# Kernel optimization log

Hardware: AMD Instinct MI355X
Metric: run time of the kernel (lower is better)

Reference implementation:

```python
import jax, jax.numpy as jnp
import numpy as np

S, B, E, H = 2048, 4, 512, 8
HD = E // H


def setup_inputs() -> dict:
    key = jax.random.key(0)
    ks = jax.random.split(key, 5)
    scale = 1.0 / np.sqrt(E)
    return {
        "query": jax.random.normal(ks[0], (S, B, E), jnp.float32),
        "key": jax.random.normal(ks[1], (S, B, E), jnp.float32),
        "value": jax.random.normal(ks[2], (S, B, E), jnp.float32),
        "in_proj_weight": jax.random.normal(ks[3], (3 * E, E), jnp.float32) * scale,
        "in_proj_bias": jnp.zeros((3 * E,), jnp.float32),
        "out_proj_weight": jax.random.normal(ks[4], (E, E), jnp.float32) * scale,
        "out_proj_bias": jnp.zeros((E,), jnp.float32),
    }


def reference(query, key, value, in_proj_weight, in_proj_bias, out_proj_weight, out_proj_bias):
    tgt_len, bsz, embed_dim = query.shape
    src_len = key.shape[0]
    # Quirk of this module: first chunk (w_qk) projects BOTH q and k; third chunk projects v.
    w_qk = in_proj_weight[:embed_dim]
    w_v = in_proj_weight[2 * embed_dim:]
    b_qk = in_proj_bias[:embed_dim]
    b_v = in_proj_bias[2 * embed_dim:]
    q = query @ w_qk.T + b_qk          # [S, B, E]
    k = key @ w_qk.T + b_qk
    v = value @ w_v.T + b_v
    # (S, B, E) -> (B*H, S, HD)
    def split_heads(x, n):
        return x.reshape(n, bsz * H, HD).transpose(1, 0, 2)
    q = split_heads(q, tgt_len) / jnp.sqrt(jnp.asarray(HD, q.dtype))
    k = split_heads(k, src_len)
    v = split_heads(v, src_len)
    scores = jnp.einsum("bqd,bkd->bqk", q, k)          # [B*H, S, S] full score matrix
    attn = jax.nn.softmax(scores, axis=-1)
    out = jnp.einsum("bqk,bkd->bqd", attn, v)          # [B*H, S, HD]
    out = out.transpose(1, 0, 2).reshape(tgt_len * bsz, embed_dim)
    out = out @ out_proj_weight.T + out_proj_bias
    return out.reshape(tgt_len, bsz, embed_dim)
```

## Files before the change

### kernel.cpp

```cpp
#include <hip/hip_runtime.h>
#include <hip/hip_bf16.h>

typedef __attribute__((ext_vector_type(8))) short s16x8;
typedef __attribute__((ext_vector_type(4))) short s16x4;
typedef __attribute__((ext_vector_type(4))) float f32x4;

#if __has_builtin(__builtin_amdgcn_exp2f)
#define EXP2F(x) __builtin_amdgcn_exp2f(x)
#else
#define EXP2F(x) exp2f(x)
#endif

#define S_LEN 2048
#define EMB   512
#define MROWS 8192

__device__ __forceinline__ float bf2f(short x) {
    union { float f; unsigned u; } z; z.u = ((unsigned)(unsigned short)x) << 16; return z.f;
}
__device__ __forceinline__ short f2bf(float f) {
    union { float f; unsigned u; } z; z.f = f;
    unsigned r = z.u + 0x7FFF + ((z.u >> 16) & 1);
    return (short)(r >> 16);
}
__device__ __forceinline__ short f2bf_fast(float f) {
    union { float f; unsigned u; } z; z.f = f;
    return (short)((z.u + 0x8000u) >> 16);
}

template<int AF32, int BF32>
__device__ __forceinline__ void gemm_mainloop(const void* __restrict__ Ag,
                                              const void* __restrict__ Bg,
                                              short* sA, short* sB,
                                              f32x4 acc[2][4], int K)
{
    const int tid  = threadIdx.x;
    const int lane = tid & 63;
    const int wv   = tid >> 6;
    const int l15  = lane & 15, quad = lane >> 4;
    const int wm   = (wv >> 1) * 32, wn = (wv & 1) * 64;

    f32x4 afr[2], bfr[2];
    s16x8 ahr, bhr;

    auto loadT = [&](const void* G, int kt, f32x4* fr, s16x8& hr, int F32) {
        if (F32) {
#pragma unroll
            for (int p = 0; p < 2; ++p) {
                int c = tid + p * 512;
                fr[p] = *(const f32x4*)((const float*)G + (size_t)(c >> 3) * K + kt + (c & 7) * 4);
            }
        } else {
            hr = *(const s16x8*)((const short*)G + (size_t)(tid >> 2) * K + kt + (tid & 3) * 8);
        }
    };
    auto commitT = [&](short* s, f32x4* fr, s16x8& hr, int F32) {
        if (F32) {
#pragma unroll
            for (int p = 0; p < 2; ++p) {
                int c = tid + p * 512;
                s16x4 o4;
                o4[0] = f2bf_fast(fr[p][0]); o4[1] = f2bf_fast(fr[p][1]);
                o4[2] = f2bf_fast(fr[p][2]); o4[3] = f2bf_fast(fr[p][3]);
                *(s16x4*)(s + c * 4) = o4;
            }
        } else {
            *(s16x8*)(s + tid * 8) = hr;
        }
    };

    loadT(Ag, 0, afr, ahr, AF32);
    loadT(Bg, 0, bfr, bhr, BF32);
    commitT(sA, afr, ahr, AF32);
    commitT(sB, bfr, bhr, BF32);
    __syncthreads();

    int cur = 0;
    for (int kt = 0; kt < K; kt += 32) {
        const int ktn = (kt + 32 < K) ? kt + 32 : 0;
        loadT(Ag, ktn, afr, ahr, AF32);
        loadT(Bg, ktn, bfr, bhr, BF32);

        const short* sAc = sA + cur * 4096;
        const short* sBc = sB + cur * 4096;
        s16x8 aF[2], bF[4];
#pragma unroll
        for (int i = 0; i < 2; ++i)
            aF[i] = *(const s16x8*)(sAc + (wm + i * 16 + l15) * 32 + quad * 8);
#pragma unroll
        for (int j = 0; j < 4; ++j)
            bF[j] = *(const s16x8*)(sBc + (wn + j * 16 + l15) * 32 + quad * 8);
#pragma unroll
        for (int i = 0; i < 2; ++i)
#pragma unroll
            for (int j = 0; j < 4; ++j)
                acc[i][j] = __builtin_amdgcn_mfma_f32_16x16x32_bf16(aF[i], bF[j], acc[i][j], 0, 0, 0);

        commitT(sA + (cur ^ 1) * 4096, afr, ahr, AF32);
        commitT(sB + (cur ^ 1) * 4096, bfr, bhr, BF32);
        __syncthreads();
        cur ^= 1;
    }
}

__global__ __launch_bounds__(512, 4) void qkv_proj(const float* __restrict__ query,
                                                   const float* __restrict__ key,
                                                   const float* __restrict__ value,
                                                   const float* __restrict__ W,
                                                   const float* __restrict__ bias,
                                                   short* __restrict__ q,
                                                   short* __restrict__ k,
                                                   short* __restrict__ vt)
{
    __shared__ __align__(16) short sA[2 * 4096], sB[2 * 4096];
    const int z = blockIdx.z;
    const float* X  = (z == 0) ? query : (z == 1) ? key : value;
    const float* Wz = W    + (z == 2 ? (size_t)1024 * EMB : 0);
    const float* bz = bias + (z == 2 ? 1024 : 0);
    const float scale = (z == 0) ? 0.125f * 1.44269504f : 1.0f;

    const int blockM = blockIdx.x * 128, blockN = blockIdx.y * 128;

    f32x4 acc[2][4];
#pragma unroll
    for (int i = 0; i < 2; ++i)
#pragma unroll
        for (int j = 0; j < 4; ++j)
            acc[i][j] = (f32x4){0.f, 0.f, 0.f, 0.f};

    gemm_mainloop<1, 1>(X + (size_t)blockM * EMB, Wz + (size_t)blockN * EMB,
                        sA, sB, acc, EMB);

    const int tid = threadIdx.x, lane = tid & 63, wv = tid >> 6;
    const int l15 = lane & 15, quad = lane >> 4;
    const int wm = (wv >> 1) * 32, wn = (wv & 1) * 64;

#pragma unroll
    for (int j = 0; j < 4; ++j) {
        int col = blockN + wn + j * 16 + l15;
        float bval = bz[col];
        int h = col >> 6, hd = col & 63;
#pragma unroll
        for (int i = 0; i < 2; ++i) {
#pragma unroll
            for (int r = 0; r < 4; ++r) {
                int row = blockM + wm + i * 16 + quad * 4 + r;
                int s = row >> 2, b = row & 3;
                float val = (acc[i][j][r] + bval) * scale;
                int bh = b * 8 + h;
                if (z == 2) {
                    vt[((size_t)(bh * 64 + hd)) * 2048 + s] = f2bf(val);
                } else {
                    short* dst = (z == 0) ? q : k;
                    dst[((size_t)(bh * 2048 + s)) * 64 + hd] = f2bf(val);
                }
            }
        }
    }
}

__global__ __launch_bounds__(256, 4) void flash_attn(const short* __restrict__ q,
                                                     const short* __restrict__ k,
                                                     const short* __restrict__ vt,
                                                     short* __restrict__ attn)
{
    __shared__ __align__(16) short sK[2][64 * 72];
    __shared__ __align__(16) short sV[2][64 * 72];
    const int bh = blockIdx.x;
    const int q0 = blockIdx.y * 64;
    const int tid = threadIdx.x, wv = tid >> 6, lane = tid & 63;
    const int l15 = lane & 15, quad = lane >> 4;

    const short* qp = q + ((size_t)(bh * 2048 + q0 + wv * 16 + l15)) * 64 + quad * 8;
    s16x8 qf0 = *(const s16x8*)qp;
    s16x8 qf1 = *(const s16x8*)(qp + 32);

    const short* kg = k  + (size_t)bh * 2048 * 64;
    const short* vg = vt + (size_t)bh * 64 * 2048;

    const int r0 = tid >> 3,          c0 = (tid & 7) * 8;
    const int r1 = (tid + 256) >> 3,  c1 = ((tid + 256) & 7) * 8;
    const int p0 = (r0 & 35) | ((r0 & 24) >> 1) | ((r0 & 4) << 2);
    const int p1 = (r1 & 35) | ((r1 & 24) >> 1) | ((r1 & 4) << 2);

    f32x4 o[4];
    float ls[4];
#pragma unroll
    for (int i = 0; i < 4; ++i) { o[i] = (f32x4){0.f, 0.f, 0.f, 0.f}; ls[i] = 0.f; }

    s16x8 ka = *(const s16x8*)(kg + (size_t)r0 * 64 + c0);
    s16x8 kb = *(const s16x8*)(kg + (size_t)r1 * 64 + c1);
    s16x8 va = *(const s16x8*)(vg + (size_t)r0 * 2048 + c0);
    s16x8 vb = *(const s16x8*)(vg + (size_t)r1 * 2048 + c1);
    *(s16x8*)(sK[0] + p0 * 72 + c0) = ka;
    *(s16x8*)(sK[0] + p1 * 72 + c1) = kb;
    *(s16x8*)(sV[0] + r0 * 72 + c0) = va;
    *(s16x8*)(sV[0] + r1 * 72 + c1) = vb;
    __syncthreads();

    int cur = 0;
    for (int kt = 0; kt < 2048; kt += 64) {
        const int ktn = (kt + 64) & 2047;
        ka = *(const s16x8*)(kg + (size_t)(ktn + r0) * 64 + c0);
        kb = *(const s16x8*)(kg + (size_t)(ktn + r1) * 64 + c1);
        va = *(const s16x8*)(vg + (size_t)r0 * 2048 + ktn + c0);
        vb = *(const s16x8*)(vg + (size_t)r1 * 2048 + ktn + c1);

        const short* Kc = sK[cur];
        const short* Vc = sV[cur];

        f32x4 sc[4];
#pragma unroll
        for (int ct = 0; ct < 4; ++ct) {
            s16x8 kf0 = *(const s16x8*)(Kc + (ct * 16 + l15) * 72 + quad * 8);
            s16x8 kf1 = *(const s16x8*)(Kc + (ct * 16 + l15) * 72 + quad * 8 + 32);
            f32x4 c = (f32x4){0.f, 0.f, 0.f, 0.f};
            c = __builtin_amdgcn_mfma_f32_16x16x32_bf16(kf0, qf0, c, 0, 0, 0);
            c = __builtin_amdgcn_mfma_f32_16x16x32_bf16(kf1, qf1, c, 0, 0, 0);
            sc[ct] = c;
        }
        s16x8 pf[2];
#pragma unroll
        for (int c = 0; c < 2; ++c)
#pragma unroll
            for (int h = 0; h < 2; ++h)
#pragma unroll
                for (int r = 0; r < 4; ++r) {
                    float p = EXP2F(sc[2 * c + h][r]);
                    ls[r] += p;
                    pf[c][h * 4 + r] = f2bf_fast(p);
                }
#pragma unroll
        for (int nt = 0; nt < 4; ++nt)
#pragma unroll
            for (int c = 0; c < 2; ++c) {
                s16x8 vf = *(const s16x8*)(Vc + (nt * 16 + l15) * 72 + c * 32 + quad * 8);
                o[nt] = __builtin_amdgcn_mfma_f32_16x16x32_bf16(pf[c], vf, o[nt], 0, 0, 0);
            }
        short* Kn = sK[cur ^ 1];
        short* Vn = sV[cur ^ 1];
        *(s16x8*)(Kn + p0 * 72 + c0) = ka;
        *(s16x8*)(Kn + p1 * 72 + c1) = kb;
        *(s16x8*)(Vn + r0 * 72 + c0) = va;
        *(s16x8*)(Vn + r1 * 72 + c1) = vb;
        __syncthreads();
        cur ^= 1;
    }

    float s = ls[0] + ls[1] + ls[2] + ls[3];
    s += __shfl_xor(s, 16, 64);
    s += __shfl_xor(s, 32, 64);
    float sinv = 1.0f / s;
    float inv[4];
#pragma unroll
    for (int r = 0; r < 4; ++r)
        inv[r] = __shfl(sinv, quad * 20 + r, 64);

    const int b = bh >> 3, h = bh & 7;
#pragma unroll
    for (int r = 0; r < 4; ++r) {
        int srow = q0 + wv * 16 + quad * 4 + r;
#pragma unroll
        for (int nt = 0; nt < 4; ++nt)
            attn[(size_t)(srow * 4 + b) * 512 + h * 64 + nt * 16 + l15] = f2bf(o[nt][r] * inv[r]);
    }
}

__global__ __launch_bounds__(512, 4) void out_proj(const short* __restrict__ attn,
                                                   const float* __restrict__ W,
                                                   const float* __restrict__ bias,
                                                   float* __restrict__ out)
{
    __shared__ __align__(16) short sA[2 * 4096], sB[2 * 4096];
    const int blockM = blockIdx.x * 128, blockN = blockIdx.y * 128;

    f32x4 acc[2][4];
#pragma unroll
    for (int i = 0; i < 2; ++i)
#pragma unroll
        for (int j = 0; j < 4; ++j)
            acc[i][j] = (f32x4){0.f, 0.f, 0.f, 0.f};

    gemm_mainloop<0, 1>(attn + (size_t)blockM * EMB, W + (size_t)blockN * EMB,
                        sA, sB, acc, EMB);

    const int tid = threadIdx.x, lane = tid & 63, wv = tid >> 6;
    const int l15 = lane & 15, quad = lane >> 4;
    const int wm = (wv >> 1) * 32, wn = (wv & 1) * 64;

#pragma unroll
    for (int j = 0; j < 4; ++j) {
        int col = blockN + wn + j * 16 + l15;
        float bval = bias[col];
#pragma unroll
        for (int i = 0; i < 2; ++i) {
#pragma unroll
            for (int r = 0; r < 4; ++r) {
                int row = blockM + wm + i * 16 + quad * 4 + r;
                out[(size_t)row * 512 + col] = acc[i][j][r] + bval;
            }
        }
    }
}

extern "C" void kernel_launch(void* const* d_in, const int* in_sizes, int n_in,
                              void* d_out, int out_size, void* d_ws, size_t ws_size,
                              hipStream_t stream)
{
    const float* query = (const float*)d_in[0];
    const float* key   = (const float*)d_in[1];
    const float* value = (const float*)d_in[2];
    const float* ipw   = (const float*)d_in[3];
    const float* ipb   = (const float*)d_in[4];
    const float* opw   = (const float*)d_in[5];
    const float* opb   = (const float*)d_in[6];
    float* out = (float*)d_out;

    const size_t NELEM = (size_t)MROWS * EMB;
    short* q    = (short*)d_ws;
    short* k    = q + NELEM;
    short* attn = k + NELEM;
    short* vt   = (short*)d_out;

    qkv_proj  <<<dim3(64, 4, 3), 512, 0, stream>>>(query, key, value, ipw, ipb, q, k, vt);
    flash_attn<<<dim3(32, 32),   256, 0, stream>>>(q, k, vt, attn);
    out_proj  <<<dim3(64, 4),    512, 0, stream>>>(attn, opw, opb, out);
}
```

Baseline: 205.5 us.

## Double query rows per attention wave and stage QKV epilogue through shared memory

```diff
diff --git a/kernel.cpp b/kernel.cpp
--- a/kernel.cpp
+++ b/kernel.cpp
@@ -112,7 +112,10 @@
                                                    short* __restrict__ k,
                                                    short* __restrict__ vt)
 {
-    __shared__ __align__(16) short sA[2 * 4096], sB[2 * 4096];
+    __shared__ __align__(16) short smem[16384];
+    short* sA = smem;
+    short* sB = smem + 8192;
+
     const int z = blockIdx.z;
     const float* X  = (z == 0) ? query : (z == 1) ? key : value;
     const float* Wz = W    + (z == 2 ? (size_t)1024 * EMB : 0);
@@ -137,29 +140,43 @@
 
 #pragma unroll
     for (int j = 0; j < 4; ++j) {
-        int col = blockN + wn + j * 16 + l15;
-        float bval = bz[col];
-        int h = col >> 6, hd = col & 63;
+        int colL = wn + j * 16 + l15;
+        float bval = bz[blockN + colL];
+        int hL = colL >> 6, hd = colL & 63;
 #pragma unroll
         for (int i = 0; i < 2; ++i) {
 #pragma unroll
             for (int r = 0; r < 4; ++r) {
-                int row = blockM + wm + i * 16 + quad * 4 + r;
-                int s = row >> 2, b = row & 3;
+                int rowL = wm + i * 16 + quad * 4 + r;
+                int b = rowL & 3, sp = rowL >> 2;
                 float val = (acc[i][j][r] + bval) * scale;
-                int bh = b * 8 + h;
-                if (z == 2) {
-                    vt[((size_t)(bh * 64 + hd)) * 2048 + s] = f2bf(val);
-                } else {
-                    short* dst = (z == 0) ? q : k;
-                    dst[((size_t)(bh * 2048 + s)) * 64 + hd] = f2bf(val);
-                }
-            }
-        }
-    }
-}
-
-__global__ __launch_bounds__(256, 4) void flash_attn(const short* __restrict__ q,
+                int idx = (z == 2) ? (((b * 2 + hL) * 64 + hd) * 32 + sp)
+                                   : (((b * 2 + hL) * 32 + sp) * 64 + hd);
+                smem[idx] = f2bf(val);
+            }
+        }
+    }
+    __syncthreads();
+
+    const s16x8* src = (const s16x8*)(smem + tid * 32);
+    if (z == 2) {
+        int b = tid >> 7, hL = (tid >> 6) & 1, hd = tid & 63;
+        int h = (blockN >> 6) + hL;
+        short* dst = vt + ((size_t)(b * 8 + h) * 64 + hd) * 2048 + (blockM >> 2);
+#pragma unroll
+        for (int u = 0; u < 4; ++u) ((s16x8*)dst)[u] = src[u];
+    } else {
+        int b = tid >> 7, hL = (tid >> 6) & 1;
+        int sp = (tid >> 1) & 31, hdh = (tid & 1) * 32;
+        int h = (blockN >> 6) + hL;
+        short* dstp = (z == 0) ? q : k;
+        short* dst = dstp + ((size_t)(b * 8 + h) * 2048 + (blockM >> 2) + sp) * 64 + hdh;
+#pragma unroll
+        for (int u = 0; u < 4; ++u) ((s16x8*)dst)[u] = src[u];
+    }
+}
+
+__global__ __launch_bounds__(256, 2) void flash_attn(const short* __restrict__ q,
                                                      const short* __restrict__ k,
                                                      const short* __restrict__ vt,
                                                      short* __restrict__ attn)
@@ -167,13 +184,17 @@
     __shared__ __align__(16) short sK[2][64 * 72];
     __shared__ __align__(16) short sV[2][64 * 72];
     const int bh = blockIdx.x;
-    const int q0 = blockIdx.y * 64;
+    const int q0 = blockIdx.y * 128;
     const int tid = threadIdx.x, wv = tid >> 6, lane = tid & 63;
     const int l15 = lane & 15, quad = lane >> 4;
 
-    const short* qp = q + ((size_t)(bh * 2048 + q0 + wv * 16 + l15)) * 64 + quad * 8;
-    s16x8 qf0 = *(const s16x8*)qp;
-    s16x8 qf1 = *(const s16x8*)(qp + 32);
+    s16x8 qf[2][2];
+#pragma unroll
+    for (int qr = 0; qr < 2; ++qr) {
+        const short* qp = q + ((size_t)(bh * 2048 + q0 + wv * 32 + qr * 16 + l15)) * 64 + quad * 8;
+        qf[qr][0] = *(const s16x8*)qp;
+        qf[qr][1] = *(const s16x8*)(qp + 32);
+    }
 
     const short* kg = k  + (size_t)bh * 2048 * 64;
     const short* vg = vt + (size_t)bh * 64 * 2048;
@@ -183,10 +204,12 @@
     const int p0 = (r0 & 35) | ((r0 & 24) >> 1) | ((r0 & 4) << 2);
     const int p1 = (r1 & 35) | ((r1 & 24) >> 1) | ((r1 & 4) << 2);
 
-    f32x4 o[4];
-    float ls[4];
-#pragma unroll
-    for (int i = 0; i < 4; ++i) { o[i] = (f32x4){0.f, 0.f, 0.f, 0.f}; ls[i] = 0.f; }
+    f32x4 o[2][4];
+    float ls[2][4];
+#pragma unroll
+    for (int qr = 0; qr < 2; ++qr)
+#pragma unroll
+        for (int i = 0; i < 4; ++i) { o[qr][i] = (f32x4){0.f, 0.f, 0.f, 0.f}; ls[qr][i] = 0.f; }
 
     s16x8 ka = *(const s16x8*)(kg + (size_t)r0 * 64 + c0);
     s16x8 kb = *(const s16x8*)(kg + (size_t)r1 * 64 + c1);
@@ -209,33 +232,40 @@
         const short* Kc = sK[cur];
         const short* Vc = sV[cur];
 
-        f32x4 sc[4];
+        f32x4 sc[2][4];
 #pragma unroll
         for (int ct = 0; ct < 4; ++ct) {
             s16x8 kf0 = *(const s16x8*)(Kc + (ct * 16 + l15) * 72 + quad * 8);
             s16x8 kf1 = *(const s16x8*)(Kc + (ct * 16 + l15) * 72 + quad * 8 + 32);
-            f32x4 c = (f32x4){0.f, 0.f, 0.f, 0.f};
-            c = __builtin_amdgcn_mfma_f32_16x16x32_bf16(kf0, qf0, c, 0, 0, 0);
-            c = __builtin_amdgcn_mfma_f32_16x16x32_bf16(kf1, qf1, c, 0, 0, 0);
-            sc[ct] = c;
-        }
-        s16x8 pf[2];
-#pragma unroll
-        for (int c = 0; c < 2; ++c)
-#pragma unroll
-            for (int h = 0; h < 2; ++h)
-#pragma unroll
-                for (int r = 0; r < 4; ++r) {
-                    float p = EXP2F(sc[2 * c + h][r]);
-                    ls[r] += p;
-                    pf[c][h * 4 + r] = f2bf_fast(p);
-                }
+#pragma unroll
+            for (int qr = 0; qr < 2; ++qr) {
+                f32x4 c = (f32x4){0.f, 0.f, 0.f, 0.f};
+                c = __builtin_amdgcn_mfma_f32_16x16x32_bf16(kf0, qf[qr][0], c, 0, 0, 0);
+                c = __builtin_amdgcn_mfma_f32_16x16x32_bf16(kf1, qf[qr][1], c, 0, 0, 0);
+                sc[qr][ct] = c;
+            }
+        }
+        s16x8 pf[2][2];
+#pragma unroll
+        for (int qr = 0; qr < 2; ++qr)
+#pragma unroll
+            for (int c = 0; c < 2; ++c)
+#pragma unroll
+                for (int h = 0; h < 2; ++h)
+#pragma unroll
+                    for (int r = 0; r < 4; ++r) {
+                        float p = EXP2F(sc[qr][2 * c + h][r]);
+                        ls[qr][r] += p;
+                        pf[qr][c][h * 4 + r] = f2bf_fast(p);
+                    }
 #pragma unroll
         for (int nt = 0; nt < 4; ++nt)
 #pragma unroll
             for (int c = 0; c < 2; ++c) {
                 s16x8 vf = *(const s16x8*)(Vc + (nt * 16 + l15) * 72 + c * 32 + quad * 8);
-                o[nt] = __builtin_amdgcn_mfma_f32_16x16x32_bf16(pf[c], vf, o[nt], 0, 0, 0);
+#pragma unroll
+                for (int qr = 0; qr < 2; ++qr)
+                    o[qr][nt] = __builtin_amdgcn_mfma_f32_16x16x32_bf16(pf[qr][c], vf, o[qr][nt], 0, 0, 0);
             }
         short* Kn = sK[cur ^ 1];
         short* Vn = sV[cur ^ 1];
@@ -247,22 +277,24 @@
         cur ^= 1;
     }
 
-    float s = ls[0] + ls[1] + ls[2] + ls[3];
-    s += __shfl_xor(s, 16, 64);
-    s += __shfl_xor(s, 32, 64);
-    float sinv = 1.0f / s;
-    float inv[4];
-#pragma unroll
-    for (int r = 0; r < 4; ++r)
-        inv[r] = __shfl(sinv, quad * 20 + r, 64);
-
     const int b = bh >> 3, h = bh & 7;
 #pragma unroll
-    for (int r = 0; r < 4; ++r) {
-        int srow = q0 + wv * 16 + quad * 4 + r;
-#pragma unroll
-        for (int nt = 0; nt < 4; ++nt)
-            attn[(size_t)(srow * 4 + b) * 512 + h * 64 + nt * 16 + l15] = f2bf(o[nt][r] * inv[r]);
+    for (int qr = 0; qr < 2; ++qr) {
+        float s = ls[qr][0] + ls[qr][1] + ls[qr][2] + ls[qr][3];
+        s += __shfl_xor(s, 16, 64);
+        s += __shfl_xor(s, 32, 64);
+        float sinv = 1.0f / s;
+        float inv[4];
+#pragma unroll
+        for (int r = 0; r < 4; ++r)
+            inv[r] = __shfl(sinv, quad * 20 + r, 64);
+#pragma unroll
+        for (int r = 0; r < 4; ++r) {
+            int srow = q0 + wv * 32 + qr * 16 + quad * 4 + r;
+#pragma unroll
+            for (int nt = 0; nt < 4; ++nt)
+                attn[(size_t)(srow * 4 + b) * 512 + h * 64 + nt * 16 + l15] = f2bf(o[qr][nt][r] * inv[r]);
+        }
     }
 }
 
@@ -323,6 +355,6 @@
     short* vt   = (short*)d_out;
 
     qkv_proj  <<<dim3(64, 4, 3), 512, 0, stream>>>(query, key, value, ipw, ipb, q, k, vt);
-    flash_attn<<<dim3(32, 32),   256, 0, stream>>>(q, k, vt, attn);
+    flash_attn<<<dim3(32, 16),   256, 0, stream>>>(q, k, vt, attn);
     out_proj  <<<dim3(64, 4),    512, 0, stream>>>(attn, opw, opb, out);
 }
```

Result: faster. 188.0 us (-8.5%).
